# Optimization experiments

Measured on AMD Instinct MI355X. Metric: run time of the kernel, lower is better.

Reference implementation:

```python
import jax, jax.numpy as jnp
import numpy as np

A, G, P, C = 250000, 64, 4096, 2
LOW, HIGH = 0.3, 0.7
BETA = 1.0 / 9.0
IMG = 800.0


def _make_boxes(key, n):
    k1, k2 = jax.random.split(key)
    xy = jax.random.uniform(k1, (n, 2), minval=0.0, maxval=IMG - 130.0)
    wh = jax.random.uniform(k2, (n, 2), minval=8.0, maxval=128.0)
    return jnp.concatenate([xy, xy + wh], axis=1)


def setup_inputs():
    ks = jax.random.split(jax.random.key(0), 11)
    return {
        "anchors": _make_boxes(ks[0], A),
        "gt_boxes": _make_boxes(ks[1], G),
        "gt_score_labels": jax.random.uniform(ks[2], (G,)),
        "gt_confidence_labels": jax.random.randint(ks[3], (G,), 0, 2),
        "objectness": jax.random.normal(ks[4], (A,)),
        "pred_bbox_deltas": jax.random.normal(ks[5], (A, 4)) * 0.1,
        "class_logits": jax.random.normal(ks[6], (P, C)),
        "box_regression": jax.random.normal(ks[7], (P, C * 4)) * 0.1,
        "roi_labels": jax.random.randint(ks[8], (P,), 0, C),
        "roi_regression_targets": jax.random.normal(ks[9], (P, 4)) * 0.1,
        "roi_scores": jax.random.uniform(ks[10], (P,)),
    }


def box_iou(a, b):
    # a: [G,4], b: [A,4] -> [G,A]
    area_a = (a[:, 2] - a[:, 0]) * (a[:, 3] - a[:, 1])
    area_b = (b[:, 2] - b[:, 0]) * (b[:, 3] - b[:, 1])
    lt = jnp.maximum(a[:, None, :2], b[None, :, :2])
    rb = jnp.minimum(a[:, None, 2:], b[None, :, 2:])
    wh = jnp.clip(rb - lt, 0.0)
    inter = wh[..., 0] * wh[..., 1]
    return inter / (area_a[:, None] + area_b[None, :] - inter)


def encode_boxes(gt, anchors):
    # torchvision BoxCoder.encode with unit weights
    aw = anchors[:, 2] - anchors[:, 0]
    ah = anchors[:, 3] - anchors[:, 1]
    acx = anchors[:, 0] + 0.5 * aw
    acy = anchors[:, 1] + 0.5 * ah
    gw = gt[:, 2] - gt[:, 0]
    gh = gt[:, 3] - gt[:, 1]
    gcx = gt[:, 0] + 0.5 * gw
    gcy = gt[:, 1] + 0.5 * gh
    return jnp.stack([(gcx - acx) / aw, (gcy - acy) / ah,
                      jnp.log(gw / aw), jnp.log(gh / ah)], axis=1)


def smooth_l1(d):
    ad = jnp.abs(d)
    return jnp.where(ad < BETA, 0.5 * d * d / BETA, ad - 0.5 * BETA)


def reference(anchors, gt_boxes, gt_score_labels, gt_confidence_labels, objectness,
              pred_bbox_deltas, class_logits, box_regression, roi_labels,
              roi_regression_targets, roi_scores):
    # ---- assign_targets_to_anchors (Matcher with low-quality matches) ----
    iou = box_iou(gt_boxes, anchors)            # [G, A]
    matched_vals = iou.max(axis=0)              # [A]
    all_matches = iou.argmax(axis=0)            # [A]
    matched_idxs = jnp.where(matched_vals < LOW, -1,
                   jnp.where(matched_vals < HIGH, -2, all_matches))
    best_per_gt = iou.max(axis=1, keepdims=True)            # [G,1]
    force = (iou == best_per_gt).any(axis=0)                # [A]
    matched_idxs = jnp.where(force, all_matches, matched_idxs)
    clamped = jnp.clip(matched_idxs, 0)
    matched_gt = gt_boxes[clamped]                          # [A,4]
    labels = (matched_idxs >= 0).astype(jnp.float32)
    labels = jnp.minimum(labels, gt_score_labels[clamped])
    labels = jnp.where(matched_idxs == -1, 0.0, labels)     # BELOW_LOW_THRESHOLD
    labels = jnp.where(matched_idxs == -2, -1.0, labels)    # BETWEEN_THRESHOLDS
    labels = jnp.where((gt_confidence_labels[clamped] == 0) & (matched_idxs >= 0), -1.0, labels)
    reg_targets = encode_boxes(matched_gt, anchors)         # [A,4]

    # ---- my_rpn_compute_loss (deterministic full pos/neg selection) ----
    pos = labels >= 1.0
    neg = labels == 0.0
    n_samp = pos.astype(jnp.float32).sum() + neg.astype(jnp.float32).sum()
    sl = smooth_l1(pred_bbox_deltas - reg_targets).sum(axis=-1)
    rpn_box_loss = (sl * pos).sum() / n_samp
    sel = pos | neg
    y = jnp.where(sel, jnp.clip(labels, 0.0, 1.0), 0.0)
    x = objectness
    bce = jnp.maximum(x, 0.0) - x * y + jnp.log1p(jnp.exp(-jnp.abs(x)))
    objectness_loss = (bce * sel).sum() / n_samp

    # ---- my_roi_loss ----
    fixed_labels = jnp.stack([1.0 - roi_scores, roi_scores], axis=1)  # [P,2]
    log_probs = jax.nn.log_softmax(class_logits, axis=1)
    classification_loss = jnp.mean(-(fixed_labels * log_probs).sum(axis=1))
    br = box_regression.reshape(P, C, 4)
    idx = jnp.broadcast_to(jnp.clip(roi_labels, 0)[:, None, None], (P, 1, 4))
    br_sel = jnp.take_along_axis(br, idx, axis=1)[:, 0]               # [P,4]
    pos_roi = (roi_labels > 0).astype(jnp.float32)
    roi_box_loss = (smooth_l1(br_sel - roi_regression_targets).sum(axis=-1) * pos_roi).sum() / P

    return jnp.stack([objectness_loss, rpn_box_loss, classification_loss, roi_box_loss])
```

## Files before the change

### kernel.cpp

```cpp
#include <hip/hip_runtime.h>
#include <hip/hip_bf16.h>
#include <math.h>

#define NA 250000
#define NG 64
#define NP 4096

#define SPAN 512
#define NB ((NA + SPAN - 1) / SPAN)
#define NBP 512
#define RBLK (NP / 256)

#define OFF_TAB    0
#define OFF_MAXARG (OFF_TAB + NG * NBP)
#define OFF_FORCE  (OFF_MAXARG + 2 * NB * SPAN)
#define FORCE_FLOATS ((NB * SPAN) / 4)
#define OFF_ROI    (OFF_FORCE + FORCE_FLOATS)
#define OFF_SUM    (OFF_ROI + RBLK * 2)


static __device__ __forceinline__ float area_of(float4 b) {
#pragma clang fp contract(off)
    return (b.z - b.x) * (b.w - b.y);
}

static __device__ __forceinline__ float iou_one(
    float gx0, float gy0, float gx1, float gy1, float ga,
    float ax0, float ay0, float ax1, float ay1, float aa)
{
#pragma clang fp contract(off)
    float ltx = fmaxf(gx0, ax0);
    float lty = fmaxf(gy0, ay0);
    float rbx = fminf(gx1, ax1);
    float rby = fminf(gy1, ay1);
    float w = fmaxf(rbx - ltx, 0.0f);
    float h = fmaxf(rby - lty, 0.0f);
    float inter = w * h;
    float uni = ga + aa - inter;
    return inter * __builtin_amdgcn_rcpf(uni);
}

static __device__ __forceinline__ float smooth_l1_f(float d) {
    const float BETA = 1.0f / 9.0f;
    float ad = fabsf(d);
    return (ad < BETA) ? (0.5f * d * d / BETA) : (ad - 0.5f * BETA);
}


__global__ __launch_bounds__(256) void kA(const float4* __restrict__ anchors,
                                          const float4* __restrict__ gt,
                                          const float* __restrict__ logits,
                                          const float* __restrict__ breg,
                                          const int* __restrict__ rlab,
                                          const float4* __restrict__ rtgt,
                                          const float* __restrict__ rsc,
                                          float* __restrict__ ws) {
    int t = threadIdx.x;
    int b = blockIdx.x;

    if (b >= NB) {
        int r = b - NB;
        if (t < NBP - NB) {
#pragma unroll
            for (int row = 0; row < 4; row++)
                ws[OFF_TAB + (4 * r + row) * NBP + NB + t] = 0.0f;
        }
        __shared__ float rbuf[4][2];
        int p = r * 256 + t;
        float l0 = logits[2 * p], l1 = logits[2 * p + 1];
        float mx = fmaxf(l0, l1);
        float lse = mx + __logf(__expf(l0 - mx) + __expf(l1 - mx));
        float s = rsc[p];
        float clsl = -((1.0f - s) * (l0 - lse) + s * (l1 - lse));

        int lbl = rlab[p];
        int cl = lbl < 0 ? 0 : lbl;
        float4 bb = *(const float4*)(breg + 8 * p + 4 * cl);
        float4 tg = rtgt[p];
        float sl = smooth_l1_f(bb.x - tg.x) + smooth_l1_f(bb.y - tg.y) +
                   smooth_l1_f(bb.z - tg.z) + smooth_l1_f(bb.w - tg.w);
        float boxl = (lbl > 0) ? sl : 0.0f;

        int lane = t & 63, w = t >> 6;
        for (int off = 32; off > 0; off >>= 1) {
            clsl += __shfl_down(clsl, off);
            boxl += __shfl_down(boxl, off);
        }
        if (lane == 0) { rbuf[w][0] = clsl; rbuf[w][1] = boxl; }
        __syncthreads();
        if (t == 0) {
            float s0 = 0.f, s1 = 0.f;
            for (int i = 0; i < 4; i++) { s0 += rbuf[i][0]; s1 += rbuf[i][1]; }
            ws[OFF_ROI + 2 * r] = s0;
            ws[OFF_ROI + 2 * r + 1] = s1;
        }
        return;
    }

    unsigned* fz = (unsigned*)(ws + OFF_FORCE);
    if (t < 128) fz[b * 128 + t] = 0u;

    int a0 = b * SPAN + t;
    int a1 = a0 + 256;
    bool ok0 = a0 < NA, ok1 = a1 < NA;
    float4 av0 = ok0 ? anchors[a0] : make_float4(0.f, 0.f, 0.f, 0.f);
    float4 av1 = ok1 ? anchors[a1] : make_float4(0.f, 0.f, 0.f, 0.f);
    float aa0 = area_of(av0);
    float aa1 = area_of(av1);

    float m[NG];
#pragma unroll
    for (int g = 0; g < NG; g++) m[g] = 0.0f;

    float max0 = -1.0f, max1 = -1.0f;
    int arg0 = 0, arg1 = 0;
#pragma unroll
    for (int g = 0; g < NG; g++) {
        float4 G = gt[g];
        float ga = area_of(G);
        float u0 = iou_one(G.x, G.y, G.z, G.w, ga, av0.x, av0.y, av0.z, av0.w, aa0);
        float u1 = iou_one(G.x, G.y, G.z, G.w, ga, av1.x, av1.y, av1.z, av1.w, aa1);
        if (u0 > max0) { max0 = u0; arg0 = g; }
        if (u1 > max1) { max1 = u1; arg1 = g; }
        m[g] = fmaxf(m[g], fmaxf(u0, u1));
    }

    float2* ma = (float2*)(ws + OFF_MAXARG);
    if (ok0) ma[a0] = make_float2(max0, __int_as_float(arg0));
    if (ok1) ma[a1] = make_float2(max1, __int_as_float(arg1));

    __shared__ float sred[4][NG];
    int lane = t & 63, w = t >> 6;
#pragma unroll
    for (int g = 0; g < NG; g++) {
        float mm = m[g];
        for (int off = 32; off > 0; off >>= 1)
            mm = fmaxf(mm, __shfl_down(mm, off));
        if (lane == 0) sred[w][g] = mm;
    }
    __syncthreads();
    if (t < NG) {
        float mm = fmaxf(fmaxf(sred[0][t], sred[1][t]),
                         fmaxf(sred[2][t], sred[3][t]));
        ws[OFF_TAB + t * NBP + b] = mm;
    }
}


__global__ __launch_bounds__(256) void kF(const float4* __restrict__ anchors,
                                          const float4* __restrict__ gt,
                                          float* __restrict__ ws) {
    __shared__ float srow[NBP];
    __shared__ float swm[4];
    __shared__ float sbest;
    __shared__ int scnt;
    __shared__ int slist[NBP];
    int t = threadIdx.x;
    int g = blockIdx.x;
    int lane = t & 63, w = t >> 6;

    const float* row = ws + OFF_TAB + g * NBP;
    float v0 = row[t], v1 = row[t + 256];
    srow[t] = v0; srow[t + 256] = v1;
    float mm = fmaxf(v0, v1);
    for (int off = 32; off > 0; off >>= 1)
        mm = fmaxf(mm, __shfl_down(mm, off));
    if (lane == 0) swm[w] = mm;
    if (t == 0) scnt = 0;
    __syncthreads();
    if (t == 0)
        sbest = fmaxf(fmaxf(swm[0], swm[1]), fmaxf(swm[2], swm[3]));
    __syncthreads();
    float best = sbest;

    if (srow[t] == best)       { int i = atomicAdd(&scnt, 1); slist[i] = t; }
    if (srow[t + 256] == best) { int i = atomicAdd(&scnt, 1); slist[i] = t + 256; }
    __syncthreads();

    float4 G = gt[g];
    float ga = area_of(G);
    char* fb = (char*)(ws + OFF_FORCE);
    int cnt = scnt;
    for (int i = 0; i < cnt; i++) {
        int s = slist[i];
        int a0 = s * SPAN + t;
        int a1 = a0 + 256;
        if (a0 < NA) {
            float4 av = anchors[a0];
            float u = iou_one(G.x, G.y, G.z, G.w, ga, av.x, av.y, av.z, av.w,
                              area_of(av));
            if (u == best) fb[a0] = 1;
        }
        if (a1 < NA) {
            float4 av = anchors[a1];
            float u = iou_one(G.x, G.y, G.z, G.w, ga, av.x, av.y, av.z, av.w,
                              area_of(av));
            if (u == best) fb[a1] = 1;
        }
    }
}


__global__ __launch_bounds__(256) void kB(const float4* __restrict__ anchors,
                                          const float* __restrict__ objness,
                                          const float4* __restrict__ pdel,
                                          const float4* __restrict__ gt,
                                          const float* __restrict__ gscore,
                                          const int* __restrict__ gconf,
                                          float* __restrict__ ws) {
    __shared__ float rbuf[4][4];
    int t = threadIdx.x;
    int b = blockIdx.x;
    int lane = t & 63, w = t >> 6;
    const float2* ma = (const float2*)(ws + OFF_MAXARG);
    const char* fb = (const char*)(ws + OFF_FORCE);

    float posf = 0.f, negf = 0.f, slpos = 0.f, bces = 0.f;
#pragma unroll
    for (int k = 0; k < 2; k++) {
        int a = b * SPAN + k * 256 + t;
        if (a >= NA) continue;
        float2 mv = ma[a];
        float maxv = mv.x;
        int arg = __float_as_int(mv.y);
        bool force = fb[a] != 0;

        int matched = (maxv < 0.3f) ? -1 : ((maxv < 0.7f) ? -2 : arg);
        if (force) matched = arg;
        int cl = matched < 0 ? 0 : matched;

        float4 Ac = gt[cl];
        float score = gscore[cl];
        int conf = gconf[cl];
        float label = (matched >= 0) ? 1.0f : 0.0f;
        label = fminf(label, score);
        if (matched == -1) label = 0.0f;
        if (matched == -2) label = -1.0f;
        if (conf == 0 && matched >= 0) label = -1.0f;

        bool pos = (label >= 1.0f);
        bool neg = (label == 0.0f);
        bool sel = pos || neg;

        float4 av = anchors[a];
        float aw = av.z - av.x, ah = av.w - av.y;
        float acx = av.x + 0.5f * aw, acy = av.y + 0.5f * ah;
        float gw = Ac.z - Ac.x, gh = Ac.w - Ac.y;
        float gcx = Ac.x + 0.5f * gw, gcy = Ac.y + 0.5f * gh;
        float t0 = (gcx - acx) / aw;
        float t1 = (gcy - acy) / ah;
        float t2 = __logf(gw / aw);
        float t3 = __logf(gh / ah);

        float4 pd = pdel[a];
        float sl = smooth_l1_f(pd.x - t0) + smooth_l1_f(pd.y - t1) +
                   smooth_l1_f(pd.z - t2) + smooth_l1_f(pd.w - t3);

        float x = objness[a];
        float y = sel ? fminf(fmaxf(label, 0.0f), 1.0f) : 0.0f;
        float bce = fmaxf(x, 0.0f) - x * y + __logf(1.0f + __expf(-fabsf(x)));

        if (pos) { posf += 1.0f; slpos += sl; }
        if (neg) negf += 1.0f;
        if (sel) bces += bce;
    }

    for (int off = 32; off > 0; off >>= 1) {
        posf  += __shfl_down(posf, off);
        negf  += __shfl_down(negf, off);
        slpos += __shfl_down(slpos, off);
        bces  += __shfl_down(bces, off);
    }
    if (lane == 0) { rbuf[w][0] = posf; rbuf[w][1] = negf; rbuf[w][2] = slpos; rbuf[w][3] = bces; }
    __syncthreads();
    if (t == 0) {
        float s0 = 0.f, s1 = 0.f, s2 = 0.f, s3 = 0.f;
        for (int i = 0; i < 4; i++) { s0 += rbuf[i][0]; s1 += rbuf[i][1]; s2 += rbuf[i][2]; s3 += rbuf[i][3]; }
        float* r = ws + OFF_SUM + 4 * b;
        r[0] = s0; r[1] = s1; r[2] = s2; r[3] = s3;
    }
}


__global__ __launch_bounds__(256) void kC(const float* __restrict__ ws,
                                          float* __restrict__ out) {
    __shared__ double sred[4][6];
    int t = threadIdx.x;
    int lane = t & 63, w = t >> 6;
    double a0 = 0, a1 = 0, a2 = 0, a3 = 0, c0 = 0, c1 = 0;
    for (int r = t; r < NB; r += 256) {
        const float4 v = *(const float4*)(ws + OFF_SUM + 4 * r);
        a0 += v.x; a1 += v.y; a2 += v.z; a3 += v.w;
    }
    if (t < RBLK) {
        c0 = ws[OFF_ROI + 2 * t];
        c1 = ws[OFF_ROI + 2 * t + 1];
    }
    for (int off = 32; off > 0; off >>= 1) {
        a0 += __shfl_down(a0, off);
        a1 += __shfl_down(a1, off);
        a2 += __shfl_down(a2, off);
        a3 += __shfl_down(a3, off);
        c0 += __shfl_down(c0, off);
        c1 += __shfl_down(c1, off);
    }
    if (lane == 0) {
        sred[w][0] = a0; sred[w][1] = a1; sred[w][2] = a2;
        sred[w][3] = a3; sred[w][4] = c0; sred[w][5] = c1;
    }
    __syncthreads();
    if (t == 0) {
        double s[6] = {0, 0, 0, 0, 0, 0};
        for (int i = 0; i < 4; i++)
            for (int j = 0; j < 6; j++) s[j] += sred[i][j];
        double n = s[0] + s[1];
        out[0] = (float)(s[3] / n);
        out[1] = (float)(s[2] / n);
        out[2] = (float)(s[4] / (double)NP);
        out[3] = (float)(s[5] / (double)NP);
    }
}

extern "C" void kernel_launch(void* const* d_in, const int* in_sizes, int n_in,
                              void* d_out, int out_size, void* d_ws, size_t ws_size,
                              hipStream_t stream) {
    const float4* anchors = (const float4*)d_in[0];
    const float4* gt      = (const float4*)d_in[1];
    const float*  gscore  = (const float*)d_in[2];
    const int*    gconf   = (const int*)d_in[3];
    const float*  objness = (const float*)d_in[4];
    const float4* pdel    = (const float4*)d_in[5];
    const float*  clog    = (const float*)d_in[6];
    const float*  breg    = (const float*)d_in[7];
    const int*    rlab    = (const int*)d_in[8];
    const float4* rtgt    = (const float4*)d_in[9];
    const float*  rsc     = (const float*)d_in[10];

    float* ws = (float*)d_ws;
    float* out = (float*)d_out;

    kA<<<NB + RBLK, 256, 0, stream>>>(anchors, gt, clog, breg, rlab, rtgt, rsc, ws);
    kF<<<NG, 256, 0, stream>>>(anchors, gt, ws);
    kB<<<NB, 256, 0, stream>>>(anchors, objness, pdel, gt, gscore, gconf, ws);
    kC<<<1, 256, 0, stream>>>(ws, out);
}
```

Baseline: 111.4 us.

## Fuse per-anchor loss into IoU kernel and apply forced matches as deltas

The per-anchor loss computation moves into the IoU/max kernel, so the max/argmax intermediate array is no longer written and the separate loss kernel is removed. The force-match kernel now recomputes the full argmax only for forced anchors and atomically adds the loss difference between the forced and the default assignment into a small accumulator, which the final reduction adds in. This cuts one launch and the global round trip of per-anchor match data. In exchange the force flags widen to one word per anchor for atomicExch deduplication, and the float atomic accumulation makes the result order-dependent.

```diff
diff --git a/kernel.cpp b/kernel.cpp
--- a/kernel.cpp
+++ b/kernel.cpp
@@ -11,12 +11,11 @@
 #define NBP 512
 #define RBLK (NP / 256)
 
-#define OFF_TAB    0
-#define OFF_MAXARG (OFF_TAB + NG * NBP)
-#define OFF_FORCE  (OFF_MAXARG + 2 * NB * SPAN)
-#define FORCE_FLOATS ((NB * SPAN) / 4)
-#define OFF_ROI    (OFF_FORCE + FORCE_FLOATS)
-#define OFF_SUM    (OFF_ROI + RBLK * 2)
+#define OFF_TAB   0
+#define OFF_FORCE (OFF_TAB + NG * NBP)
+#define OFF_ROI   (OFF_FORCE + NB * SPAN)
+#define OFF_ACC   (OFF_ROI + RBLK * 2)
+#define OFF_SUM   (OFF_ACC + 4)
 
 
 static __device__ __forceinline__ float area_of(float4 b) {
@@ -46,9 +45,57 @@
     return (ad < BETA) ? (0.5f * d * d / BETA) : (ad - 0.5f * BETA);
 }
 
+static __device__ __forceinline__ int matched_of(float maxv, int arg) {
+    return (maxv < 0.3f) ? -1 : ((maxv < 0.7f) ? -2 : arg);
+}
+
+static __device__ __forceinline__ void add_losses(
+    int matched, const float4* __restrict__ gt,
+    const float* __restrict__ gscore, const int* __restrict__ gconf,
+    float4 av, float4 pd, float x,
+    float& posf, float& negf, float& slpos, float& bces)
+{
+    int cl = matched < 0 ? 0 : matched;
+    float4 Ac = gt[cl];
+    float score = gscore[cl];
+    int conf = gconf[cl];
+    float label = (matched >= 0) ? 1.0f : 0.0f;
+    label = fminf(label, score);
+    if (matched == -1) label = 0.0f;
+    if (matched == -2) label = -1.0f;
+    if (conf == 0 && matched >= 0) label = -1.0f;
+
+    bool pos = (label >= 1.0f);
+    bool neg = (label == 0.0f);
+    bool sel = pos || neg;
+
+    float aw = av.z - av.x, ah = av.w - av.y;
+    float acx = av.x + 0.5f * aw, acy = av.y + 0.5f * ah;
+    float gw = Ac.z - Ac.x, gh = Ac.w - Ac.y;
+    float gcx = Ac.x + 0.5f * gw, gcy = Ac.y + 0.5f * gh;
+    float t0 = (gcx - acx) / aw;
+    float t1 = (gcy - acy) / ah;
+    float t2 = __logf(gw / aw);
+    float t3 = __logf(gh / ah);
+
+    float sl = smooth_l1_f(pd.x - t0) + smooth_l1_f(pd.y - t1) +
+               smooth_l1_f(pd.z - t2) + smooth_l1_f(pd.w - t3);
+
+    float y = sel ? fminf(fmaxf(label, 0.0f), 1.0f) : 0.0f;
+    float bce = fmaxf(x, 0.0f) - x * y + __logf(1.0f + __expf(-fabsf(x)));
+
+    if (pos) { posf += 1.0f; slpos += sl; }
+    if (neg) negf += 1.0f;
+    if (sel) bces += bce;
+}
+
 
 __global__ __launch_bounds__(256) void kA(const float4* __restrict__ anchors,
                                           const float4* __restrict__ gt,
+                                          const float* __restrict__ gscore,
+                                          const int* __restrict__ gconf,
+                                          const float* __restrict__ objness,
+                                          const float4* __restrict__ pdel,
                                           const float* __restrict__ logits,
                                           const float* __restrict__ breg,
                                           const int* __restrict__ rlab,
@@ -57,6 +104,7 @@
                                           float* __restrict__ ws) {
     int t = threadIdx.x;
     int b = blockIdx.x;
+    int lane = t & 63, w = t >> 6;
 
     if (b >= NB) {
         int r = b - NB;
@@ -65,6 +113,8 @@
             for (int row = 0; row < 4; row++)
                 ws[OFF_TAB + (4 * r + row) * NBP + NB + t] = 0.0f;
         }
+        if (r == 0 && t >= 32 && t < 36) ws[OFF_ACC + (t - 32)] = 0.0f;
+
         __shared__ float rbuf[4][2];
         int p = r * 256 + t;
         float l0 = logits[2 * p], l1 = logits[2 * p + 1];
@@ -81,7 +131,6 @@
                    smooth_l1_f(bb.z - tg.z) + smooth_l1_f(bb.w - tg.w);
         float boxl = (lbl > 0) ? sl : 0.0f;
 
-        int lane = t & 63, w = t >> 6;
         for (int off = 32; off > 0; off >>= 1) {
             clsl += __shfl_down(clsl, off);
             boxl += __shfl_down(boxl, off);
@@ -97,8 +146,9 @@
         return;
     }
 
-    unsigned* fz = (unsigned*)(ws + OFF_FORCE);
-    if (t < 128) fz[b * 128 + t] = 0u;
+    unsigned* fw = (unsigned*)(ws + OFF_FORCE);
+    fw[b * SPAN + t] = 0u;
+    fw[b * SPAN + 256 + t] = 0u;
 
     int a0 = b * SPAN + t;
     int a1 = a0 + 256;
@@ -107,11 +157,12 @@
     float4 av1 = ok1 ? anchors[a1] : make_float4(0.f, 0.f, 0.f, 0.f);
     float aa0 = area_of(av0);
     float aa1 = area_of(av1);
+    float4 pd0 = ok0 ? pdel[a0] : make_float4(0.f, 0.f, 0.f, 0.f);
+    float4 pd1 = ok1 ? pdel[a1] : make_float4(0.f, 0.f, 0.f, 0.f);
+    float x0 = ok0 ? objness[a0] : 0.0f;
+    float x1 = ok1 ? objness[a1] : 0.0f;
 
     float m[NG];
-#pragma unroll
-    for (int g = 0; g < NG; g++) m[g] = 0.0f;
-
     float max0 = -1.0f, max1 = -1.0f;
     int arg0 = 0, arg1 = 0;
 #pragma unroll
@@ -122,15 +173,10 @@
         float u1 = iou_one(G.x, G.y, G.z, G.w, ga, av1.x, av1.y, av1.z, av1.w, aa1);
         if (u0 > max0) { max0 = u0; arg0 = g; }
         if (u1 > max1) { max1 = u1; arg1 = g; }
-        m[g] = fmaxf(m[g], fmaxf(u0, u1));
-    }
-
-    float2* ma = (float2*)(ws + OFF_MAXARG);
-    if (ok0) ma[a0] = make_float2(max0, __int_as_float(arg0));
-    if (ok1) ma[a1] = make_float2(max1, __int_as_float(arg1));
+        m[g] = fmaxf(fmaxf(u0, u1), 0.0f);
+    }
 
     __shared__ float sred[4][NG];
-    int lane = t & 63, w = t >> 6;
 #pragma unroll
     for (int g = 0; g < NG; g++) {
         float mm = m[g];
@@ -144,11 +190,37 @@
                          fmaxf(sred[2][t], sred[3][t]));
         ws[OFF_TAB + t * NBP + b] = mm;
     }
+
+    float posf = 0.f, negf = 0.f, slpos = 0.f, bces = 0.f;
+    if (ok0) add_losses(matched_of(max0, arg0), gt, gscore, gconf,
+                        av0, pd0, x0, posf, negf, slpos, bces);
+    if (ok1) add_losses(matched_of(max1, arg1), gt, gscore, gconf,
+                        av1, pd1, x1, posf, negf, slpos, bces);
+
+    __shared__ float rbuf[4][4];
+    for (int off = 32; off > 0; off >>= 1) {
+        posf  += __shfl_down(posf, off);
+        negf  += __shfl_down(negf, off);
+        slpos += __shfl_down(slpos, off);
+        bces  += __shfl_down(bces, off);
+    }
+    if (lane == 0) { rbuf[w][0] = posf; rbuf[w][1] = negf; rbuf[w][2] = slpos; rbuf[w][3] = bces; }
+    __syncthreads();
+    if (t == 0) {
+        float s0 = 0.f, s1 = 0.f, s2 = 0.f, s3 = 0.f;
+        for (int i = 0; i < 4; i++) { s0 += rbuf[i][0]; s1 += rbuf[i][1]; s2 += rbuf[i][2]; s3 += rbuf[i][3]; }
+        float* r = ws + OFF_SUM + 4 * b;
+        r[0] = s0; r[1] = s1; r[2] = s2; r[3] = s3;
+    }
 }
 
 
 __global__ __launch_bounds__(256) void kF(const float4* __restrict__ anchors,
                                           const float4* __restrict__ gt,
+                                          const float* __restrict__ gscore,
+                                          const int* __restrict__ gconf,
+                                          const float* __restrict__ objness,
+                                          const float4* __restrict__ pdel,
                                           float* __restrict__ ws) {
     __shared__ float srow[NBP];
     __shared__ float swm[4];
@@ -179,105 +251,43 @@
 
     float4 G = gt[g];
     float ga = area_of(G);
-    char* fb = (char*)(ws + OFF_FORCE);
+    unsigned* fw = (unsigned*)(ws + OFF_FORCE);
+    float* acc = ws + OFF_ACC;
     int cnt = scnt;
     for (int i = 0; i < cnt; i++) {
         int s = slist[i];
-        int a0 = s * SPAN + t;
-        int a1 = a0 + 256;
-        if (a0 < NA) {
-            float4 av = anchors[a0];
-            float u = iou_one(G.x, G.y, G.z, G.w, ga, av.x, av.y, av.z, av.w,
-                              area_of(av));
-            if (u == best) fb[a0] = 1;
+#pragma unroll
+        for (int k = 0; k < 2; k++) {
+            int a = s * SPAN + k * 256 + t;
+            if (a >= NA) continue;
+            float4 av = anchors[a];
+            float aa = area_of(av);
+            float u = iou_one(G.x, G.y, G.z, G.w, ga,
+                              av.x, av.y, av.z, av.w, aa);
+            if (u != best) continue;
+            if (atomicExch(&fw[a], 1u) != 0u) continue;
+            float maxv = -1.0f;
+            int arg = 0;
+            for (int j = 0; j < NG; j++) {
+                float4 Gj = gt[j];
+                float gaj = area_of(Gj);
+                float uj = iou_one(Gj.x, Gj.y, Gj.z, Gj.w, gaj,
+                                   av.x, av.y, av.z, av.w, aa);
+                if (uj > maxv) { maxv = uj; arg = j; }
+            }
+            int mu = matched_of(maxv, arg);
+            if (mu == arg) continue;
+            float4 pd = pdel[a];
+            float x = objness[a];
+            float pu = 0.f, nu = 0.f, su = 0.f, bu = 0.f;
+            float pf = 0.f, nf = 0.f, sf = 0.f, bf = 0.f;
+            add_losses(mu, gt, gscore, gconf, av, pd, x, pu, nu, su, bu);
+            add_losses(arg, gt, gscore, gconf, av, pd, x, pf, nf, sf, bf);
+            atomicAdd(&acc[0], pf - pu);
+            atomicAdd(&acc[1], nf - nu);
+            atomicAdd(&acc[2], sf - su);
+            atomicAdd(&acc[3], bf - bu);
         }
-        if (a1 < NA) {
-            float4 av = anchors[a1];
-            float u = iou_one(G.x, G.y, G.z, G.w, ga, av.x, av.y, av.z, av.w,
-                              area_of(av));
-            if (u == best) fb[a1] = 1;
-        }
-    }
-}
-
-
-__global__ __launch_bounds__(256) void kB(const float4* __restrict__ anchors,
-                                          const float* __restrict__ objness,
-                                          const float4* __restrict__ pdel,
-                                          const float4* __restrict__ gt,
-                                          const float* __restrict__ gscore,
-                                          const int* __restrict__ gconf,
-                                          float* __restrict__ ws) {
-    __shared__ float rbuf[4][4];
-    int t = threadIdx.x;
-    int b = blockIdx.x;
-    int lane = t & 63, w = t >> 6;
-    const float2* ma = (const float2*)(ws + OFF_MAXARG);
-    const char* fb = (const char*)(ws + OFF_FORCE);
-
-    float posf = 0.f, negf = 0.f, slpos = 0.f, bces = 0.f;
-#pragma unroll
-    for (int k = 0; k < 2; k++) {
-        int a = b * SPAN + k * 256 + t;
-        if (a >= NA) continue;
-        float2 mv = ma[a];
-        float maxv = mv.x;
-        int arg = __float_as_int(mv.y);
-        bool force = fb[a] != 0;
-
-        int matched = (maxv < 0.3f) ? -1 : ((maxv < 0.7f) ? -2 : arg);
-        if (force) matched = arg;
-        int cl = matched < 0 ? 0 : matched;
-
-        float4 Ac = gt[cl];
-        float score = gscore[cl];
-        int conf = gconf[cl];
-        float label = (matched >= 0) ? 1.0f : 0.0f;
-        label = fminf(label, score);
-        if (matched == -1) label = 0.0f;
-        if (matched == -2) label = -1.0f;
-        if (conf == 0 && matched >= 0) label = -1.0f;
-
-        bool pos = (label >= 1.0f);
-        bool neg = (label == 0.0f);
-        bool sel = pos || neg;
-
-        float4 av = anchors[a];
-        float aw = av.z - av.x, ah = av.w - av.y;
-        float acx = av.x + 0.5f * aw, acy = av.y + 0.5f * ah;
-        float gw = Ac.z - Ac.x, gh = Ac.w - Ac.y;
-        float gcx = Ac.x + 0.5f * gw, gcy = Ac.y + 0.5f * gh;
-        float t0 = (gcx - acx) / aw;
-        float t1 = (gcy - acy) / ah;
-        float t2 = __logf(gw / aw);
-        float t3 = __logf(gh / ah);
-
-        float4 pd = pdel[a];
-        float sl = smooth_l1_f(pd.x - t0) + smooth_l1_f(pd.y - t1) +
-                   smooth_l1_f(pd.z - t2) + smooth_l1_f(pd.w - t3);
-
-        float x = objness[a];
-        float y = sel ? fminf(fmaxf(label, 0.0f), 1.0f) : 0.0f;
-        float bce = fmaxf(x, 0.0f) - x * y + __logf(1.0f + __expf(-fabsf(x)));
-
-        if (pos) { posf += 1.0f; slpos += sl; }
-        if (neg) negf += 1.0f;
-        if (sel) bces += bce;
-    }
-
-    for (int off = 32; off > 0; off >>= 1) {
-        posf  += __shfl_down(posf, off);
-        negf  += __shfl_down(negf, off);
-        slpos += __shfl_down(slpos, off);
-        bces  += __shfl_down(bces, off);
-    }
-    if (lane == 0) { rbuf[w][0] = posf; rbuf[w][1] = negf; rbuf[w][2] = slpos; rbuf[w][3] = bces; }
-    __syncthreads();
-    if (t == 0) {
-        float s0 = 0.f, s1 = 0.f, s2 = 0.f, s3 = 0.f;
-        for (int i = 0; i < 4; i++) { s0 += rbuf[i][0]; s1 += rbuf[i][1]; s2 += rbuf[i][2]; s3 += rbuf[i][3]; }
-        float* r = ws + OFF_SUM + 4 * b;
-        r[0] = s0; r[1] = s1; r[2] = s2; r[3] = s3;
     }
 }
 
@@ -313,6 +323,10 @@
         double s[6] = {0, 0, 0, 0, 0, 0};
         for (int i = 0; i < 4; i++)
             for (int j = 0; j < 6; j++) s[j] += sred[i][j];
+        s[0] += (double)ws[OFF_ACC + 0];
+        s[1] += (double)ws[OFF_ACC + 1];
+        s[2] += (double)ws[OFF_ACC + 2];
+        s[3] += (double)ws[OFF_ACC + 3];
         double n = s[0] + s[1];
         out[0] = (float)(s[3] / n);
         out[1] = (float)(s[2] / n);
@@ -339,8 +353,8 @@
     float* ws = (float*)d_ws;
     float* out = (float*)d_out;
 
-    kA<<<NB + RBLK, 256, 0, stream>>>(anchors, gt, clog, breg, rlab, rtgt, rsc, ws);
-    kF<<<NG, 256, 0, stream>>>(anchors, gt, ws);
-    kB<<<NB, 256, 0, stream>>>(anchors, objness, pdel, gt, gscore, gconf, ws);
+    kA<<<NB + RBLK, 256, 0, stream>>>(anchors, gt, gscore, gconf, objness, pdel,
+                                      clog, breg, rlab, rtgt, rsc, ws);
+    kF<<<NG, 256, 0, stream>>>(anchors, gt, gscore, gconf, objness, pdel, ws);
     kC<<<1, 256, 0, stream>>>(ws, out);
 }
```

Result: slower. 115.0 us (+3.3%).
